# Kernel tuning notes

Hardware: AMD Instinct MI355X
Metric: run time of the kernel (lower is better)

The kernel has to match this reference:

```python
import jax, jax.numpy as jnp
import numpy as np

D_MODEL = 1024
N_HEAD = 16
D_K = D_MODEL // N_HEAD


def setup_inputs() -> dict:
    key = jax.random.key(0)
    ks = jax.random.split(key, 9)
    s = 1.0 / np.sqrt(D_MODEL)
    return {
        "x": jax.random.normal(ks[0], (2, 2048, D_MODEL), dtype=jnp.float32),
        "Wq": jax.random.uniform(ks[1], (D_MODEL, D_MODEL), jnp.float32, -s, s),
        "bq": jax.random.uniform(ks[2], (D_MODEL,), jnp.float32, -s, s),
        "Wk": jax.random.uniform(ks[3], (D_MODEL, D_MODEL), jnp.float32, -s, s),
        "bk": jax.random.uniform(ks[4], (D_MODEL,), jnp.float32, -s, s),
        "Wv": jax.random.uniform(ks[5], (D_MODEL, D_MODEL), jnp.float32, -s, s),
        "bv": jax.random.uniform(ks[6], (D_MODEL,), jnp.float32, -s, s),
        "Wo": jax.random.uniform(ks[7], (D_MODEL, D_MODEL), jnp.float32, -s, s),
        "bo": jax.random.uniform(ks[8], (D_MODEL,), jnp.float32, -s, s),
    }


def reference(x, Wq, bq, Wk, bk, Wv, bv, Wo, bo):
    B, S, D = x.shape
    # linear projections (torch Linear: x @ W.T + b)
    q = x @ Wq.T + bq
    k = x @ Wk.T + bk
    v = x @ Wv.T + bv
    # split heads: [B, H, S, d_k]
    q = q.reshape(B, S, N_HEAD, D_K).transpose(0, 2, 1, 3)
    k = k.reshape(B, S, N_HEAD, D_K).transpose(0, 2, 1, 3)
    v = v.reshape(B, S, N_HEAD, D_K).transpose(0, 2, 1, 3)
    scores = jnp.einsum("bhqd,bhkd->bhqk", q, k) / np.sqrt(D_K).astype(jnp.float32)
    attn = jax.nn.softmax(scores, axis=-1)
    out = jnp.einsum("bhqk,bhkd->bhqd", attn, v)
    out = out.transpose(0, 2, 1, 3).reshape(B, S, D)
    return out @ Wo.T + bo
```

## Files before the change

### kernel.cpp

```cpp
#include <hip/hip_runtime.h>
#include <hip/hip_bf16.h>


typedef unsigned short u16;
typedef __attribute__((ext_vector_type(4))) unsigned short u16x4;
typedef __attribute__((ext_vector_type(8))) short short8;
typedef __attribute__((ext_vector_type(4))) float f32x4;

__device__ __forceinline__ u16 f2bf(float f) {
  __bf16 b = (__bf16)f;
  return __builtin_bit_cast(unsigned short, b);
}

__device__ __forceinline__ f32x4 mfma_bf16(short8 a, short8 b, f32x4 c) {
  return __builtin_amdgcn_mfma_f32_16x16x32_bf16(a, b, c, 0, 0, 0);
}

#define GLL16(gp, lp) __builtin_amdgcn_global_load_lds( \
    (const __attribute__((address_space(1))) void*)(gp), \
    (__attribute__((address_space(3))) void*)(lp), 16, 0, 0)

#define QSCALE 0.18033688011112042f

__global__ __launch_bounds__(256) void cast_all(
    const float* __restrict__ x,
    const float* __restrict__ wq, const float* __restrict__ wk,
    const float* __restrict__ wv, const float* __restrict__ wo,
    u16* __restrict__ xb, u16* __restrict__ wqb, u16* __restrict__ wkb,
    u16* __restrict__ wvb, u16* __restrict__ wob)
{
  const int z = blockIdx.z;
  const float* s; u16* d; int n4;
  if (z == 0)      { s = x;  d = xb;  n4 = 1048576; }
  else if (z == 1) { s = wq; d = wqb; n4 = 262144; }
  else if (z == 2) { s = wk; d = wkb; n4 = 262144; }
  else if (z == 3) { s = wv; d = wvb; n4 = 262144; }
  else             { s = wo; d = wob; n4 = 262144; }
  int i = blockIdx.x * 256 + threadIdx.x;
  if (i >= n4) return;
  float4 v = ((const float4*)s)[i];
  u16x4 o; o[0] = f2bf(v.x); o[1] = f2bf(v.y); o[2] = f2bf(v.z); o[3] = f2bf(v.w);
  ((u16x4*)d)[i] = o;
}

__device__ __forceinline__ void gemm_core(const u16* __restrict__ A,
                                          const u16* __restrict__ B,
                                          u16* sA, u16* sB, f32x4 acc[4][4])
{
  const int tid = threadIdx.x;
  const int lane = tid & 63, wave = tid >> 6;
  const int wr = wave >> 1, wc = wave & 1;
  const int m0 = blockIdx.y * 128, n0 = blockIdx.x * 128;
  const u16* ga = A + (size_t)(m0 + (tid >> 2)) * 1024 + (tid & 3) * 8;
  const u16* gb = B + (size_t)(n0 + (tid >> 2)) * 1024 + (tid & 3) * 8;
  u16* la0 = sA + wave * 512;          u16* la1 = sA + 2048 + wave * 512;
  u16* lb0 = sB + wave * 512;          u16* lb1 = sB + 2048 + wave * 512;
  const int rl = lane & 15, kg = (lane >> 4) * 8;

  for (int k0 = 0; k0 < 1024; k0 += 32) {
    GLL16(ga + k0,             la0);
    GLL16(ga + 64 * 1024 + k0, la1);
    GLL16(gb + k0,             lb0);
    GLL16(gb + 64 * 1024 + k0, lb1);
    __syncthreads();
    short8 af[4], bf_[4];
#pragma unroll
    for (int m = 0; m < 4; ++m) af[m]  = *(const short8*)&sA[(wr * 64 + m * 16 + rl) * 32 + kg];
#pragma unroll
    for (int n = 0; n < 4; ++n) bf_[n] = *(const short8*)&sB[(wc * 64 + n * 16 + rl) * 32 + kg];
#pragma unroll
    for (int m = 0; m < 4; ++m)
#pragma unroll
      for (int n = 0; n < 4; ++n)
        acc[m][n] = mfma_bf16(af[m], bf_[n], acc[m][n]);
    __syncthreads();
  }
}

__global__ __launch_bounds__(256) void gemm_qkv(
    const u16* __restrict__ X,
    const u16* __restrict__ Wqb, const u16* __restrict__ Wkb, const u16* __restrict__ Wvb,
    const float* __restrict__ bq, const float* __restrict__ bk, const float* __restrict__ bv,
    u16* __restrict__ Qo, u16* __restrict__ Ko, u16* __restrict__ Vt)
{
  __shared__ u16 sA[4096], sB[4096];
  const int z = blockIdx.z;
  const u16* W = (z == 0) ? Wqb : (z == 1) ? Wkb : Wvb;
  const float* bias = (z == 0) ? bq : (z == 1) ? bk : bv;

  f32x4 acc[4][4];
#pragma unroll
  for (int m = 0; m < 4; ++m)
#pragma unroll
    for (int n = 0; n < 4; ++n) acc[m][n] = (f32x4){0.f, 0.f, 0.f, 0.f};

  gemm_core(X, W, sA, sB, acc);

  const int lane = threadIdx.x & 63, wave = threadIdx.x >> 6;
  const int wr = wave >> 1, wc = wave & 1;
  const int m0 = blockIdx.y * 128, n0 = blockIdx.x * 128;
  const int rl = lane & 15, rg = (lane >> 4) * 4;

  if (z < 2) {
    u16* dst = (z == 0) ? Qo : Ko;
    const float cs = (z == 0) ? QSCALE : 1.0f;
#pragma unroll
    for (int n = 0; n < 4; ++n) {
      int col = n0 + wc * 64 + n * 16 + rl;
      float bb = bias[col];
#pragma unroll
      for (int m = 0; m < 4; ++m) {
        int row0 = m0 + wr * 64 + m * 16 + rg;
#pragma unroll
        for (int r = 0; r < 4; ++r)
          dst[(size_t)(row0 + r) * 1024 + col] = f2bf((acc[m][n][r] + bb) * cs);
      }
    }
  } else {
#pragma unroll
    for (int n = 0; n < 4; ++n) {
      int col = n0 + wc * 64 + n * 16 + rl;
      float bb = bias[col];
#pragma unroll
      for (int m = 0; m < 4; ++m) {
        int row0 = m0 + wr * 64 + m * 16 + rg;
        int bidx = row0 >> 11, sl = row0 & 2047;
        u16x4 pk;
#pragma unroll
        for (int r = 0; r < 4; ++r) pk[r] = f2bf(acc[m][n][r] + bb);
        *(u16x4*)&Vt[((size_t)(bidx * 1024 + col)) * 2048 + sl] = pk;
      }
    }
  }
}

__global__ __launch_bounds__(256) void gemm_out(
    const u16* __restrict__ Ob, const u16* __restrict__ Wob,
    const float* __restrict__ bo, float* __restrict__ Out)
{
  __shared__ u16 sA[4096], sB[4096];
  f32x4 acc[4][4];
#pragma unroll
  for (int m = 0; m < 4; ++m)
#pragma unroll
    for (int n = 0; n < 4; ++n) acc[m][n] = (f32x4){0.f, 0.f, 0.f, 0.f};

  gemm_core(Ob, Wob, sA, sB, acc);

  const int lane = threadIdx.x & 63, wave = threadIdx.x >> 6;
  const int wr = wave >> 1, wc = wave & 1;
  const int m0 = blockIdx.y * 128, n0 = blockIdx.x * 128;
  const int rl = lane & 15, rg = (lane >> 4) * 4;
#pragma unroll
  for (int n = 0; n < 4; ++n) {
    int col = n0 + wc * 64 + n * 16 + rl;
    float bb = bo[col];
#pragma unroll
    for (int m = 0; m < 4; ++m) {
      int row0 = m0 + wr * 64 + m * 16 + rg;
#pragma unroll
      for (int r = 0; r < 4; ++r)
        Out[(size_t)(row0 + r) * 1024 + col] = acc[m][n][r] + bb;
    }
  }
}

__global__ __launch_bounds__(256) void attn_fwd(
    const u16* __restrict__ Q, const u16* __restrict__ K,
    const u16* __restrict__ Vt, u16* __restrict__ O)
{
  __shared__ u16 sK[2][64][64];
  __shared__ u16 sV[2][64][64];

  const int tid = threadIdx.x, lane = tid & 63, wave = tid >> 6;
  const int rl = lane & 15, g = lane >> 4;

  const int bflat = blockIdx.x;
  const int xcd = bflat & 7, j = bflat >> 3;
  const int bh = xcd * 4 + (j >> 4);
  const int qchunk = j & 15;
  const int b = bh >> 4, h = bh & 15;
  const int qbase = qchunk * 128 + wave * 32;

  const u16* Qp = Q + (size_t)(b * 2048 + qbase) * 1024 + h * 64;
  const u16* Kp = K + (size_t)(b * 2048) * 1024 + h * 64;
  const u16* Vp = Vt + (size_t)(bh * 64) * 2048;

  short8 qf[2][2];
#pragma unroll
  for (int qg = 0; qg < 2; ++qg)
#pragma unroll
    for (int hf = 0; hf < 2; ++hf)
      qf[qg][hf] = *(const short8*)&Qp[(size_t)(qg * 16 + rl) * 1024 + hf * 32 + g * 8];

  const int keyperm = 8 * (rl >> 2) + (rl & 3);
  const int swzK8 = (((rl & 3) | (((rl >> 2) & 1) << 2))) * 8;
  const int swzV8 = (rl & 7) * 8;

  const int srow = lane >> 3;
  const int feK = (((lane & 7) * 8) ^ ((srow & 3) * 8));
  const int feV = (((lane & 7) ^ srow) * 8);

  f32x4 oacc[2][4];
  f32x4 lacc[2];
#pragma unroll
  for (int qg = 0; qg < 2; ++qg) {
    lacc[qg] = (f32x4){0.f, 0.f, 0.f, 0.f};
#pragma unroll
    for (int dg = 0; dg < 4; ++dg) oacc[qg][dg] = (f32x4){0.f, 0.f, 0.f, 0.f};
  }
  float mrun[2] = {-INFINITY, -INFINITY};

  const short8 ONES = {0x3F80, 0x3F80, 0x3F80, 0x3F80,
                       0x3F80, 0x3F80, 0x3F80, 0x3F80};

  auto stage = [&](int nb, int kt) {
#pragma unroll
    for (int c = 0; c < 2; ++c) {
      const int chunk = wave * 2 + c;
      const int grow = chunk * 8 + srow;
      GLL16(Kp + (size_t)(kt + grow) * 1024 + (feK ^ (c * 32)),
            &sK[nb][chunk * 8][0]);
      GLL16(Vp + (size_t)grow * 2048 + kt + feV,
            &sV[nb][chunk * 8][0]);
    }
  };

  auto proc_sub = [&](int nb, int sub) {
    short8 kf[2][2];
#pragma unroll
    for (int t = 0; t < 2; ++t) {
      const int r = sub * 32 + keyperm + 4 * t;
#pragma unroll
      for (int hf = 0; hf < 2; ++hf)
        kf[t][hf] = *(const short8*)&sK[nb][r][(hf * 32 + g * 8) ^ swzK8];
    }
    short8 vf[4];
#pragma unroll
    for (int dg = 0; dg < 4; ++dg)
      vf[dg] = *(const short8*)&sV[nb][dg * 16 + rl][(sub * 32 + g * 8) ^ swzV8];

    f32x4 sc[2][2];
    __builtin_amdgcn_s_setprio(1);
#pragma unroll
    for (int qg = 0; qg < 2; ++qg)
#pragma unroll
      for (int t = 0; t < 2; ++t) {
        f32x4 a = (f32x4){0.f, 0.f, 0.f, 0.f};
        a = mfma_bf16(kf[t][0], qf[qg][0], a);
        a = mfma_bf16(kf[t][1], qf[qg][1], a);
        sc[qg][t] = a;
      }
    __builtin_amdgcn_s_setprio(0);

    short8 pb[2];
#pragma unroll
    for (int qg = 0; qg < 2; ++qg) {
      float p2[8];
#pragma unroll
      for (int t = 0; t < 2; ++t)
#pragma unroll
        for (int r = 0; r < 4; ++r) p2[t * 4 + r] = sc[qg][t][r];
      float a0 = fmaxf(fmaxf(p2[0], p2[1]), p2[2]);
      float a1 = fmaxf(fmaxf(p2[3], p2[4]), p2[5]);
      float a2 = fmaxf(p2[6], p2[7]);
      float tm = fmaxf(fmaxf(a0, a1), a2);
      if (!__all(tm <= mrun[qg] + 8.0f)) {
        tm = fmaxf(tm, __shfl_xor(tm, 16));
        tm = fmaxf(tm, __shfl_xor(tm, 32));
        float mnew = fmaxf(mrun[qg], tm);
        float sfac = __builtin_amdgcn_exp2f(mrun[qg] - mnew);
        mrun[qg] = mnew;
#pragma unroll
        for (int dg = 0; dg < 4; ++dg)
#pragma unroll
          for (int r = 0; r < 4; ++r) oacc[qg][dg][r] *= sfac;
        lacc[qg][0] *= sfac;
      }
      short8 pk;
#pragma unroll
      for (int j2 = 0; j2 < 8; ++j2)
        pk[j2] = (short)f2bf(__builtin_amdgcn_exp2f(p2[j2] - mrun[qg]));
      pb[qg] = pk;
      lacc[qg] = mfma_bf16(ONES, pb[qg], lacc[qg]);
    }
    __builtin_amdgcn_s_setprio(1);
#pragma unroll
    for (int dg = 0; dg < 4; ++dg)
#pragma unroll
      for (int qg = 0; qg < 2; ++qg)
        oacc[qg][dg] = mfma_bf16(vf[dg], pb[qg], oacc[qg][dg]);
    __builtin_amdgcn_s_setprio(0);
  };

  stage(0, 0);
  __syncthreads();
  for (int kt = 0; kt < 2048; kt += 128) {
    stage(1, kt + 64);
    proc_sub(0, 0);
    proc_sub(0, 1);
    __syncthreads();
    if (kt + 128 < 2048) stage(0, kt + 128);
    proc_sub(1, 0);
    proc_sub(1, 1);
    __syncthreads();
  }

#pragma unroll
  for (int qg = 0; qg < 2; ++qg) {
    float inv = 1.0f / lacc[qg][0];
    int qrow = qbase + qg * 16 + rl;
    u16* op = O + (size_t)(b * 2048 + qrow) * 1024 + h * 64;
#pragma unroll
    for (int dg = 0; dg < 4; ++dg) {
      u16x4 pk;
#pragma unroll
      for (int r = 0; r < 4; ++r) pk[r] = f2bf(oacc[qg][dg][r] * inv);
      *(u16x4*)&op[dg * 16 + g * 4] = pk;
    }
  }
}

extern "C" void kernel_launch(void* const* d_in, const int* in_sizes, int n_in,
                              void* d_out, int out_size, void* d_ws, size_t ws_size,
                              hipStream_t stream) {
  const float* x  = (const float*)d_in[0];
  const float* Wq = (const float*)d_in[1];
  const float* bq = (const float*)d_in[2];
  const float* Wk = (const float*)d_in[3];
  const float* bk = (const float*)d_in[4];
  const float* Wv = (const float*)d_in[5];
  const float* bv = (const float*)d_in[6];
  const float* Wo = (const float*)d_in[7];
  const float* bo = (const float*)d_in[8];

  char* ws = (char*)d_ws;
  const size_t MB = 1024 * 1024;
  u16* Xb  = (u16*)(ws + 0 * MB);
  u16* Wqb = (u16*)(ws + 8 * MB);
  u16* Wkb = (u16*)(ws + 10 * MB);
  u16* Wvb = (u16*)(ws + 12 * MB);
  u16* Wob = (u16*)(ws + 14 * MB);
  u16* Qb  = (u16*)(ws + 16 * MB);
  u16* Kb  = (u16*)(ws + 24 * MB);
  u16* Vtb = (u16*)(ws + 32 * MB);
  u16* Ob  = (u16*)(ws + 40 * MB);

  cast_all<<<dim3(4096, 1, 5), 256, 0, stream>>>(x, Wq, Wk, Wv, Wo,
                                                 Xb, Wqb, Wkb, Wvb, Wob);
  gemm_qkv<<<dim3(8, 32, 3), 256, 0, stream>>>(Xb, Wqb, Wkb, Wvb,
                                               bq, bk, bv, Qb, Kb, Vtb);
  attn_fwd<<<dim3(512), 256, 0, stream>>>(Qb, Kb, Vtb, Ob);
  gemm_out<<<dim3(8, 32), 256, 0, stream>>>(Ob, Wob, bo, (float*)d_out);
}
```

Baseline: 120.4 us.

## Split attention key range across wave pairs with LDS merge of partial softmax

Attention blocks grow from 256 to 512 threads. Each pair of waves handles the same 32 query rows but takes different halves of the key sequence, with the key/value staging remapped so each tile holds two 32-key slices from separate halves. At the end the partial output, running max and sum are merged through a shared-memory buffer using the rescaled online-softmax combine. The aim is more waves in flight to hide latency, at the cost of extra LDS (about 36KB), a merge step, and higher register pressure under launch_bounds(512,4).

```diff
diff --git a/kernel.cpp b/kernel.cpp
--- a/kernel.cpp
+++ b/kernel.cpp
@@ -165,22 +165,24 @@
   }
 }
 
-__global__ __launch_bounds__(256) void attn_fwd(
+__global__ __launch_bounds__(512, 4) void attn_fwd(
     const u16* __restrict__ Q, const u16* __restrict__ K,
     const u16* __restrict__ Vt, u16* __restrict__ O)
 {
   __shared__ u16 sK[2][64][64];
   __shared__ u16 sV[2][64][64];
+  __shared__ float mbuf[9216];
 
   const int tid = threadIdx.x, lane = tid & 63, wave = tid >> 6;
   const int rl = lane & 15, g = lane >> 4;
+  const int qslot = wave >> 1, half = wave & 1;
 
   const int bflat = blockIdx.x;
   const int xcd = bflat & 7, j = bflat >> 3;
   const int bh = xcd * 4 + (j >> 4);
-  const int qchunk = j & 15;
+  const int qidx = j & 15;
   const int b = bh >> 4, h = bh & 15;
-  const int qbase = qchunk * 128 + wave * 32;
+  const int qbase = qidx * 128 + qslot * 32;
 
   const u16* Qp = Q + (size_t)(b * 2048 + qbase) * 1024 + h * 64;
   const u16* Kp = K + (size_t)(b * 2048) * 1024 + h * 64;
@@ -195,11 +197,10 @@
 
   const int keyperm = 8 * (rl >> 2) + (rl & 3);
   const int swzK8 = (((rl & 3) | (((rl >> 2) & 1) << 2))) * 8;
-  const int swzV8 = (rl & 7) * 8;
-
-  const int srow = lane >> 3;
-  const int feK = (((lane & 7) * 8) ^ ((srow & 3) * 8));
-  const int feV = (((lane & 7) ^ srow) * 8);
+
+  const int krow = tid >> 3;
+  const int feK = (((tid & 7) ^ (krow & 3)) * 8) ^ ((wave & 1) * 32);
+  const int gp  = (tid & 7) ^ (krow & 7);
 
   f32x4 oacc[2][4];
   f32x4 lacc[2];
@@ -214,42 +215,37 @@
   const short8 ONES = {0x3F80, 0x3F80, 0x3F80, 0x3F80,
                        0x3F80, 0x3F80, 0x3F80, 0x3F80};
 
-  auto stage = [&](int nb, int kt) {
-#pragma unroll
-    for (int c = 0; c < 2; ++c) {
-      const int chunk = wave * 2 + c;
-      const int grow = chunk * 8 + srow;
-      GLL16(Kp + (size_t)(kt + grow) * 1024 + (feK ^ (c * 32)),
-            &sK[nb][chunk * 8][0]);
-      GLL16(Vp + (size_t)grow * 2048 + kt + feV,
-            &sV[nb][chunk * 8][0]);
-    }
+  auto stage = [&](int nb, int t) {
+    GLL16(Kp + (size_t)(((krow >> 5) << 10) + t * 32 + (krow & 31)) * 1024 + feK,
+          &sK[nb][wave * 8][0]);
+    GLL16(Vp + (size_t)krow * 2048 + ((gp >> 2) << 10) + t * 32 + (gp & 3) * 8,
+          &sV[nb][wave * 8][0]);
   };
 
-  auto proc_sub = [&](int nb, int sub) {
+  auto proc = [&](int nb) {
     short8 kf[2][2];
 #pragma unroll
-    for (int t = 0; t < 2; ++t) {
-      const int r = sub * 32 + keyperm + 4 * t;
+    for (int t2 = 0; t2 < 2; ++t2) {
+      const int r = half * 32 + keyperm + 4 * t2;
 #pragma unroll
       for (int hf = 0; hf < 2; ++hf)
-        kf[t][hf] = *(const short8*)&sK[nb][r][(hf * 32 + g * 8) ^ swzK8];
+        kf[t2][hf] = *(const short8*)&sK[nb][r][(hf * 32 + g * 8) ^ swzK8];
     }
     short8 vf[4];
 #pragma unroll
     for (int dg = 0; dg < 4; ++dg)
-      vf[dg] = *(const short8*)&sV[nb][dg * 16 + rl][(sub * 32 + g * 8) ^ swzV8];
+      vf[dg] = *(const short8*)&sV[nb][dg * 16 + rl][(((half << 2) | g) ^ (rl & 7)) * 8];
 
     f32x4 sc[2][2];
     __builtin_amdgcn_s_setprio(1);
 #pragma unroll
     for (int qg = 0; qg < 2; ++qg)
 #pragma unroll
-      for (int t = 0; t < 2; ++t) {
+      for (int t2 = 0; t2 < 2; ++t2) {
         f32x4 a = (f32x4){0.f, 0.f, 0.f, 0.f};
-        a = mfma_bf16(kf[t][0], qf[qg][0], a);
-        a = mfma_bf16(kf[t][1], qf[qg][1], a);
-        sc[qg][t] = a;
+        a = mfma_bf16(kf[t2][0], qf[qg][0], a);
+        a = mfma_bf16(kf[t2][1], qf[qg][1], a);
+        sc[qg][t2] = a;
       }
     __builtin_amdgcn_s_setprio(0);
 
@@ -258,9 +254,9 @@
     for (int qg = 0; qg < 2; ++qg) {
       float p2[8];
 #pragma unroll
-      for (int t = 0; t < 2; ++t)
-#pragma unroll
-        for (int r = 0; r < 4; ++r) p2[t * 4 + r] = sc[qg][t][r];
+      for (int t2 = 0; t2 < 2; ++t2)
+#pragma unroll
+        for (int r = 0; r < 4; ++r) p2[t2 * 4 + r] = sc[qg][t2][r];
       float a0 = fmaxf(fmaxf(p2[0], p2[1]), p2[2]);
       float a1 = fmaxf(fmaxf(p2[3], p2[4]), p2[5]);
       float a2 = fmaxf(p2[6], p2[7]);
@@ -295,28 +291,48 @@
 
   stage(0, 0);
   __syncthreads();
-  for (int kt = 0; kt < 2048; kt += 128) {
-    stage(1, kt + 64);
-    proc_sub(0, 0);
-    proc_sub(0, 1);
+  for (int t = 0; t < 32; t += 2) {
+    stage(1, t + 1);
+    proc(0);
     __syncthreads();
-    if (kt + 128 < 2048) stage(0, kt + 128);
-    proc_sub(1, 0);
-    proc_sub(1, 1);
+    if (t + 2 < 32) stage(0, t + 2);
+    proc(1);
     __syncthreads();
   }
 
-#pragma unroll
-  for (int qg = 0; qg < 2; ++qg) {
-    float inv = 1.0f / lacc[qg][0];
-    int qrow = qbase + qg * 16 + rl;
-    u16* op = O + (size_t)(b * 2048 + qrow) * 1024 + h * 64;
-#pragma unroll
-    for (int dg = 0; dg < 4; ++dg) {
-      u16x4 pk;
-#pragma unroll
-      for (int r = 0; r < 4; ++r) pk[r] = f2bf(oacc[qg][dg][r] * inv);
-      *(u16x4*)&op[dg * 16 + g * 4] = pk;
+  const int mb = (qslot * 64 + lane) * 36;
+  if (half == 1) {
+#pragma unroll
+    for (int qg = 0; qg < 2; ++qg) {
+#pragma unroll
+      for (int dg = 0; dg < 4; ++dg)
+#pragma unroll
+        for (int r = 0; r < 4; ++r)
+          mbuf[mb + qg * 18 + dg * 4 + r] = oacc[qg][dg][r];
+      mbuf[mb + qg * 18 + 16] = mrun[qg];
+      mbuf[mb + qg * 18 + 17] = lacc[qg][0];
+    }
+  }
+  __syncthreads();
+  if (half == 0) {
+#pragma unroll
+    for (int qg = 0; qg < 2; ++qg) {
+      float m2 = mbuf[mb + qg * 18 + 16];
+      float l2 = mbuf[mb + qg * 18 + 17];
+      float mnew = fmaxf(mrun[qg], m2);
+      float fa = __builtin_amdgcn_exp2f(mrun[qg] - mnew);
+      float fb = __builtin_amdgcn_exp2f(m2 - mnew);
+      float inv = 1.0f / (lacc[qg][0] * fa + l2 * fb);
+      int qrow = qbase + qg * 16 + rl;
+      u16* op = O + (size_t)(b * 2048 + qrow) * 1024 + h * 64;
+#pragma unroll
+      for (int dg = 0; dg < 4; ++dg) {
+        u16x4 pk;
+#pragma unroll
+        for (int r = 0; r < 4; ++r)
+          pk[r] = f2bf((oacc[qg][dg][r] * fa + mbuf[mb + qg * 18 + dg * 4 + r] * fb) * inv);
+        *(u16x4*)&op[dg * 16 + g * 4] = pk;
+      }
     }
   }
 }
@@ -350,6 +366,6 @@
                                                  Xb, Wqb, Wkb, Wvb, Wob);
   gemm_qkv<<<dim3(8, 32, 3), 256, 0, stream>>>(Xb, Wqb, Wkb, Wvb,
                                                bq, bk, bv, Qb, Kb, Vtb);
-  attn_fwd<<<dim3(512), 256, 0, stream>>>(Qb, Kb, Vtb, Ob);
+  attn_fwd<<<dim3(512), 512, 0, stream>>>(Qb, Kb, Vtb, Ob);
   gemm_out<<<dim3(8, 32), 256, 0, stream>>>(Ob, Wob, bo, (float*)d_out);
 }
```

Result: faster. 116.1 us (-3.6%).
